# Kernel tuning notes

Measured on AMD Instinct MI355X. Metric: run time of the kernel, lower is better.

Reference implementation:

```python
import jax, jax.numpy as jnp
import numpy as np

DEPTH = 6
D_IN = 512
D_OUT = 256
NUM_NODES = 2 ** (DEPTH + 1) - 1   # 127
NUM_LEAVES = 2 ** (DEPTH + 1)      # 128
BATCH = 8192
EPS = 0.01


def _routes(depth):
    num_nodes = 2 ** (depth + 1) - 1
    num_leaves = 2 ** (depth + 1)
    idxs = np.zeros((num_leaves, depth + 1), np.int32)
    sides = np.zeros((num_leaves, depth + 1), np.int32)
    for i in range(num_leaves):
        temp, temp_sides = [], []
        leaf_idx = num_nodes + i
        for _ in range(depth):
            parent_idx = (leaf_idx - 1) // 2
            temp.append(parent_idx)
            temp_sides.append(1 if (leaf_idx - 1) % 2 == 0 else 0)
            leaf_idx = parent_idx
        temp_sides.append(1 if (leaf_idx - 1) % 2 == 0 else 0)
        temp.append(0)
        idxs[i] = temp[::-1]
        sides[i] = temp_sides[::-1]
    return idxs, sides


def _l2norm(v, axis):
    # matches torch F.normalize (eps=1e-12)
    n = jnp.sqrt(jnp.sum(v * v, axis=axis, keepdims=True))
    return v / jnp.maximum(n, 1e-12)


def setup_inputs() -> dict:
    key = jax.random.key(0)
    ks = jax.random.split(key, 6)
    D1 = D_IN + 1  # pre-network output dim
    x = jax.random.normal(ks[0], (BATCH, D_IN), jnp.float32)
    # pre_network Linear(D_IN, D_IN+1)
    W_pre = jax.random.normal(ks[1], (D1, D_IN), jnp.float32) * (1.0 / np.sqrt(D_IN))
    b_pre = jax.random.normal(ks[2], (D1,), jnp.float32) * 0.01
    # node hyperplanes [num_nodes, D1]
    right_w = jax.random.normal(ks[3], (NUM_NODES, D1), jnp.float32)
    # leaves Linear(D1, out*num_leaves)
    W_leaf = jax.random.normal(ks[4], (D_OUT * NUM_LEAVES, D1), jnp.float32) * (1.0 / np.sqrt(D1))
    b_leaf = jax.random.normal(ks[5], (D_OUT * NUM_LEAVES,), jnp.float32) * 0.01
    idxs, sides = _routes(DEPTH)
    return {
        "x": x, "W_pre": W_pre, "b_pre": b_pre, "right_w": right_w,
        "W_leaf": W_leaf, "b_leaf": b_leaf,
        "route_idx": jnp.asarray(idxs, jnp.int32),
        "route_side": jnp.asarray(sides, jnp.int32),
    }


def reference(x, W_pre, b_pre, right_w, W_leaf, b_leaf, route_idx, route_side):
    b = x.shape[0]
    # pre-network: Linear + ReLU  -> [b, D1]
    h = jax.nn.relu(x @ W_pre.T + b_pre)
    # node probabilities (cosine-similarity routing)
    nx = _l2norm(h, axis=1)                  # [b, D1]
    nw = _l2norm(right_w, axis=1)            # [N, D1]
    right = nx @ nw.T                        # [b, N]
    right_dist = (1.0 - right) / 2.0
    left_dist = 1.0 - right_dist
    # all_indices [2, N, b]
    all_ind = jnp.stack([right_dist.T, left_dist.T], axis=0)
    # gather route probs -> [L, depth+1, b]
    probs = all_ind[route_side, route_idx]
    log_probs = jnp.log(jnp.clip(probs, EPS, 1.0 - EPS))
    leaves_logp = jnp.sum(log_probs, axis=1)        # [L, b]
    s_w = jnp.exp(leaves_logp)                       # [L, b]
    entropy = -jnp.sum(s_w * leaves_logp, axis=0)    # [b]
    max_entropy = (NUM_LEAVES / DEPTH) * jnp.log(jnp.float32(DEPTH))
    entropy_loss = entropy / max_entropy
    # all leaf outputs at once -> [b, L, out]
    results = (h @ W_leaf.T + b_leaf).reshape(b, NUM_LEAVES, D_OUT)
    # NOTE: original multiplies by (randn(1) + 1 + entropy_loss.mean());
    # the randn(1) term is fixed to 0 for a deterministic reference.
    scale = 1.0 + jnp.mean(entropy_loss)
    out = jnp.sum(results * scale * s_w.T[:, :, None], axis=1)  # [b, out]
    return out
```

## Files before the change

kernel.cpp:

```cpp
#include <hip/hip_runtime.h>

typedef _Float16 f16;
typedef unsigned short u16;
typedef unsigned int u32;
typedef _Float16 f16x8 __attribute__((ext_vector_type(8)));
typedef float f32x4 __attribute__((ext_vector_type(4)));

union F16x8U { f16x8 v; uint4 q; u16 us[8]; f16 h[8]; };
union HBits { f16 f; u16 u; };

#define GLD16(g, l)                                                        \
  __builtin_amdgcn_global_load_lds(                                        \
      (const __attribute__((address_space(1))) void*)(g),                  \
      (__attribute__((address_space(3))) void*)(l), 16, 0, 0)

__global__ void kcvt_x(const float* __restrict__ x, f16* __restrict__ xo) {
  int i = (blockIdx.x * 256 + threadIdx.x) << 3;
  float4 a = *(const float4*)(x + i);
  float4 b = *(const float4*)(x + i + 4);
  F16x8U u;
  u.h[0] = (f16)a.x; u.h[1] = (f16)a.y; u.h[2] = (f16)a.z; u.h[3] = (f16)a.w;
  u.h[4] = (f16)b.x; u.h[5] = (f16)b.y; u.h[6] = (f16)b.z; u.h[7] = (f16)b.w;
  *(uint4*)(xo + i) = u.q;
}

__global__ void kcvt_wpre(const float* __restrict__ w, f16* __restrict__ wo) {
  int e = (blockIdx.x * 256 + threadIdx.x) << 2;
  int row = e >> 9, col = e & 511;
  union { uint2 q; f16 h[4]; } u;
  if (row < 513) {
    float4 v = *(const float4*)(w + (size_t)row * 512 + col);
    u.h[0] = (f16)v.x; u.h[1] = (f16)v.y; u.h[2] = (f16)v.z; u.h[3] = (f16)v.w;
  } else {
    u.h[0] = u.h[1] = u.h[2] = u.h[3] = (f16)0.0f;
  }
  *(uint2*)(wo + e) = u.q;
}

__global__ void kcvt_rw(const float* __restrict__ rwsrc, f16* __restrict__ ro) {
  int e = (blockIdx.x * 256 + threadIdx.x) << 2;
  int row = e / 576, c0 = e - row * 576;
  union { uint2 q; f16 h[4]; } u;
#pragma unroll
  for (int i = 0; i < 4; ++i) {
    int c = c0 + i;
    float v = (row < 127 && c < 513) ? rwsrc[(size_t)row * 513 + c] : 0.0f;
    u.h[i] = (f16)v;
  }
  *(uint2*)(ro + e) = u.q;
}

__global__ void kcvt_wleaf(const float* __restrict__ wl, const float* __restrict__ bl,
                           f16* __restrict__ wo) {
  int e = (blockIdx.x * 256 + threadIdx.x) << 3;
  int row = e / 544, c0 = e - row * 544;
  const float* src = wl + (size_t)row * 513 + c0;
  F16x8U u;
#pragma unroll
  for (int i = 0; i < 8; ++i) {
    int c = c0 + i;
    float v = (c < 513) ? src[i] : ((c == 513) ? bl[row] : 0.0f);
    u.h[i] = (f16)v;
  }
  *(uint4*)(wo + e) = u.q;
}

template <int MODE>
__global__ __launch_bounds__(256, 2) void kgemm(
    const f16* __restrict__ A, const f16* __restrict__ B,
    const float* __restrict__ bias, void* __restrict__ C,
    int NK, int astr, int bstr) {
  __shared__ alignas(16) f16 al[2][128 * 32];
  __shared__ alignas(16) f16 bl[2][64 * 40];
  const int tid = threadIdx.x, lane = tid & 63, wid = tid >> 6;
  const int wm = wid >> 1, wn = wid & 1;
  const int brow = blockIdx.x << 7, bcol = blockIdx.y << 6;

  int arow[2], aseg[2];
#pragma unroll
  for (int i = 0; i < 2; ++i) { int c = i * 256 + tid; arow[i] = c >> 2; aseg[i] = c & 3; }
  int br0 = tid / 5, bs0 = tid - br0 * 5;
  int c1 = 256 + lane;
  int br1 = c1 / 5, bs1 = c1 - br1 * 5;

  f32x4 acc[4][2];
#pragma unroll
  for (int mf = 0; mf < 4; ++mf)
#pragma unroll
    for (int nf = 0; nf < 2; ++nf)
#pragma unroll
      for (int j = 0; j < 4; ++j) acc[mf][nf][j] = 0.0f;

  auto stage = [&](int kc, int bf) {
    int kcol = kc << 5;
#pragma unroll
    for (int i = 0; i < 2; ++i) {
      f16* ldsb = &al[bf][(i * 256 + (wid << 6)) << 3];
      GLD16(A + (size_t)(brow + arow[i]) * astr + kcol + (aseg[i] << 3), ldsb);
    }
    {
      f16* ldsb = &bl[bf][(wid << 6) << 3];
      GLD16(B + (size_t)(bcol + br0) * bstr + kcol + (bs0 < 4 ? (bs0 << 3) : 0), ldsb);
    }
    if (wid == 0) {
      f16* ldsb = &bl[bf][256 << 3];
      GLD16(B + (size_t)(bcol + br1) * bstr + kcol + (bs1 < 4 ? (bs1 << 3) : 0), ldsb);
    }
  };

  stage(0, 0);
  __syncthreads();
  int cur = 0;
  for (int kc = 0; kc < NK; ++kc) {
    if (kc + 1 < NK) stage(kc + 1, cur ^ 1);
    f16x8 af[4], bfm[2];
#pragma unroll
    for (int mf = 0; mf < 4; ++mf)
      af[mf] = *(const f16x8*)&al[cur][((wm << 6) + (mf << 4) + (lane & 15)) * 32 + ((lane >> 4) << 3)];
#pragma unroll
    for (int nf = 0; nf < 2; ++nf)
      bfm[nf] = *(const f16x8*)&bl[cur][((wn << 5) + (nf << 4) + (lane & 15)) * 40 + ((lane >> 4) << 3)];
#pragma unroll
    for (int mf = 0; mf < 4; ++mf)
#pragma unroll
      for (int nf = 0; nf < 2; ++nf)
        acc[mf][nf] = __builtin_amdgcn_mfma_f32_16x16x32_f16(af[mf], bfm[nf], acc[mf][nf], 0, 0, 0);
    __syncthreads();
    cur ^= 1;
  }

#pragma unroll
  for (int mf = 0; mf < 4; ++mf) {
#pragma unroll
    for (int nf = 0; nf < 2; ++nf) {
      int gcol = bcol + (wn << 5) + (nf << 4) + (lane & 15);
      int gr0 = brow + (wm << 6) + (mf << 4) + ((lane >> 4) << 2);
      if (MODE == 0) {
        float bv = (gcol < 513) ? bias[gcol] : 0.0f;
#pragma unroll
        for (int j = 0; j < 4; ++j) {
          float v = fmaxf(acc[mf][nf][j] + bv, 0.0f);
          ((f16*)C)[(size_t)(gr0 + j) * 576 + gcol] = (gcol == 513) ? (f16)1.0f : (f16)v;
        }
      } else {
#pragma unroll
        for (int j = 0; j < 4; ++j)
          ((float*)C)[(size_t)(gr0 + j) * 128 + gcol] = acc[mf][nf][j];
      }
    }
  }
}

__global__ void khnorm(const f16* __restrict__ hf, float* __restrict__ ihn) {
  int row = (blockIdx.x << 2) + (threadIdx.x >> 6);
  int lane = threadIdx.x & 63;
  float s = 0.0f;
  for (int c = lane; c < 513; c += 64) {
    float v = (float)hf[(size_t)row * 576 + c];
    s += v * v;
  }
  for (int o = 32; o; o >>= 1) s += __shfl_down(s, o);
  if (!lane) ihn[row] = 1.0f / fmaxf(sqrtf(s), 1e-12f);
}

__global__ void kinvrw(const float* __restrict__ rw, float* __restrict__ irw) {
  int j = (blockIdx.x << 2) + (threadIdx.x >> 6);
  if (j >= 127) return;
  int lane = threadIdx.x & 63;
  float s = 0.0f;
  for (int d = lane; d < 513; d += 64) {
    float v = rw[(size_t)j * 513 + d];
    s += v * v;
  }
  for (int o = 32; o; o >>= 1) s += __shfl_down(s, o);
  if (!lane) irw[j] = 1.0f / fmaxf(sqrtf(s), 1e-12f);
}

__global__ void kroute(const float* __restrict__ G, const float* __restrict__ ihn,
                       const float* __restrict__ irw, u16* __restrict__ swh,
                       float* __restrict__ entp) {
  int b = blockIdx.x * 256 + threadIdx.x;
  float ih = ihn[b];
  const float* g = G + (size_t)b * 128;
  float ent = 0.0f;
  size_t wbase = (size_t)(b & ~127) + (((size_t)b & 15) << 3) + ((b >> 4) & 7);
  for (int l = 0; l < 128; ++l) {
    int n = 0;
    float lp = 0.0f;
#pragma unroll
    for (int k = 6; k >= 0; --k) {
      int bit = (l >> k) & 1;
      float cs = g[n] * ih * irw[n];
      float pr = bit ? 0.5f * (1.0f - cs) : 0.5f * (1.0f + cs);
      pr = fminf(fmaxf(pr, 0.01f), 0.99f);
      lp += __logf(pr);
      n = 2 * n + 1 + bit;
    }
    float sw = __expf(lp);
    ent -= sw * lp;
    HBits hb; hb.f = (f16)sw;
    swh[(size_t)l * 8192 + wbase] = hb.u;
  }
  for (int o = 32; o; o >>= 1) ent += __shfl_down(ent, o);
  __shared__ float red[4];
  if (!(threadIdx.x & 63)) red[threadIdx.x >> 6] = ent;
  __syncthreads();
  if (!threadIdx.x) atomicAdd(entp, red[0] + red[1] + red[2] + red[3]);
}

__global__ __launch_bounds__(512, 2) void kbig(
    const f16* __restrict__ hf, const f16* __restrict__ wp,
    const u16* __restrict__ swh, const float* __restrict__ entp,
    float* __restrict__ out) {
  __shared__ alignas(16) u16 slds[16384];
  __shared__ alignas(16) f16 blds[4][8192];

  const int tid = threadIdx.x;
  const int lane = tid & 63, wid = tid >> 6;
  const int lh = wid >> 2;
  const int wm = (wid >> 1) & 1;
  const int wn = wid & 1;

  const int d = blockIdx.x;
  const int ob = (d >> 1) & 3;
  const int mb = ((d & 1) << 5) | (d >> 3);
  const int brow = mb << 7;
  const int ocol = ob << 6;

#pragma unroll
  for (int i = 0; i < 4; ++i) {
    int c = i * 512 + tid;
    int l = c >> 4, q = (c & 15) << 3;
    GLD16(swh + ((size_t)l << 13) + brow + q, slds + ((i * 512 + (wid << 6)) << 3));
  }

  int pb[2];
#pragma unroll
  for (int i = 0; i < 2; ++i) {
    int c = i * 512 + tid;
    int leaf = c >> 8, r = (c >> 2) & 63, sl = c & 3;
    int ss = sl ^ ((r >> 2) & 3);
    pb[i] = (leaf * 256 + ocol + r) * 544 + (ss << 3);
  }
  auto stageB = [&](int s) {
    const f16* src = wp + (size_t)(s & 31) * 557056 + ((s >> 5) << 5);
    f16* bb = blds[s & 3];
#pragma unroll
    for (int i = 0; i < 2; ++i)
      GLD16(src + pb[i], bb + ((i * 512 + (wid << 6)) << 3));
  };

  stageB(0);
  stageB(1);

  f32x4 acc[4][2];
#pragma unroll
  for (int mf = 0; mf < 4; ++mf)
#pragma unroll
    for (int nf = 0; nf < 2; ++nf)
#pragma unroll
      for (int j = 0; j < 4; ++j) acc[mf][nf][j] = 0.0f;

  f16x8 afr[4];
  const f16* abase = hf + (size_t)(brow + (wm << 6) + (lane & 15)) * 576 + ((lane >> 4) << 3);
  int boff[2];
#pragma unroll
  for (int nf = 0; nf < 2; ++nf) {
    int r = (wn << 5) + (nf << 4) + (lane & 15);
    int s4 = (lane >> 4) ^ ((r >> 2) & 3);
    boff[nf] = (r << 5) + (s4 << 3);
  }
  const int soff = ((lane & 15) << 3) + (wm << 2);

  for (int s = 0; s < 544; ++s) {
    const int kc = s >> 5, lg = s & 31;
    if (lg == 0) {
      const f16* ap = abase + (kc << 5);
#pragma unroll
      for (int mf = 0; mf < 4; ++mf)
        afr[mf] = *(const f16x8*)(ap + (size_t)(mf << 4) * 576);
    }
    __builtin_amdgcn_sched_barrier(0);
    if (s + 2 < 544) stageB(s + 2);
    __builtin_amdgcn_sched_barrier(0);
    if (s + 2 < 544)      asm volatile("s_waitcnt vmcnt(4)" ::: "memory");
    else if (s == 542)    asm volatile("s_waitcnt vmcnt(2)" ::: "memory");
    else                  asm volatile("s_waitcnt vmcnt(0)" ::: "memory");
    __builtin_amdgcn_s_barrier();
    __builtin_amdgcn_sched_barrier(0);

    const f16* bb = blds[s & 3];
    __builtin_amdgcn_s_setprio(1);
#pragma unroll
    for (int ls = 0; ls < 2; ++ls) {
      const int l = (lg << 2) + (lh << 1) + ls;
      uint2 sq = *(const uint2*)(slds + (l << 7) + soff);
      const f16* bl0 = bb + ((l & 3) << 11);
      f16x8 bfr0 = *(const f16x8*)(bl0 + boff[0]);
      f16x8 bfr1 = *(const f16x8*)(bl0 + boff[1]);
      u16 sc[4] = {(u16)(sq.x & 0xffffu), (u16)(sq.x >> 16),
                   (u16)(sq.y & 0xffffu), (u16)(sq.y >> 16)};
#pragma unroll
      for (int mf = 0; mf < 4; ++mf) {
        HBits hb; hb.u = sc[mf];
        f16x8 as = afr[mf] * hb.f;
        acc[mf][0] = __builtin_amdgcn_mfma_f32_16x16x32_f16(as, bfr0, acc[mf][0], 0, 0, 0);
        acc[mf][1] = __builtin_amdgcn_mfma_f32_16x16x32_f16(as, bfr1, acc[mf][1], 0, 0, 0);
      }
    }
    __builtin_amdgcn_s_setprio(0);
    __builtin_amdgcn_sched_barrier(0);
  }

  float* rb = (float*)&blds[0][0];
  const int p = (wm << 1) | wn;
  if (lh == 1) {
    float* wbase = rb + ((p << 6) + lane) * 36;
#pragma unroll
    for (int mf = 0; mf < 4; ++mf)
#pragma unroll
      for (int nf = 0; nf < 2; ++nf)
        *(f32x4*)(wbase + (((mf << 1) + nf) << 2)) = acc[mf][nf];
  }
  __syncthreads();
  if (lh == 0) {
    const float* rbase = rb + ((p << 6) + lane) * 36;
    float ent = *entp;
    float scale = 1.0f + ent / (8192.0f * (128.0f / 6.0f) * logf(6.0f));
    const int cc0 = ocol + (wn << 5) + (lane & 15);
#pragma unroll
    for (int mf = 0; mf < 4; ++mf) {
#pragma unroll
      for (int nf = 0; nf < 2; ++nf) {
        f32x4 o = acc[mf][nf] + *(const f32x4*)(rbase + (((mf << 1) + nf) << 2));
        int r0 = brow + (wm << 6) + (mf << 4) + ((lane >> 4) << 2);
        int cc = cc0 + (nf << 4);
#pragma unroll
        for (int j = 0; j < 4; ++j)
          out[(size_t)(r0 + j) * 256 + cc] = scale * o[j];
      }
    }
  }
}

extern "C" void kernel_launch(void* const* d_in, const int* in_sizes, int n_in,
                              void* d_out, int out_size, void* d_ws, size_t ws_size,
                              hipStream_t stream) {
  const float* x     = (const float*)d_in[0];
  const float* wpre  = (const float*)d_in[1];
  const float* bpre  = (const float*)d_in[2];
  const float* rw    = (const float*)d_in[3];
  const float* wleaf = (const float*)d_in[4];
  const float* bleaf = (const float*)d_in[5];
  float* out = (float*)d_out;

  char* ws = (char*)d_ws;
  constexpr size_t O_ENT = 0;
  constexpr size_t O_XO  = 256;
  constexpr size_t O_WPO = O_XO  + 8388608;
  constexpr size_t O_RWO = O_WPO + 589824;
  constexpr size_t O_IRW = O_RWO + 147456;
  constexpr size_t O_HO  = O_IRW + 512;
  constexpr size_t O_IHN = O_HO  + 9437184;
  constexpr size_t O_G   = O_IHN + 32768;
  constexpr size_t O_SWH = O_G   + 4194304;
  constexpr size_t O_WPK = O_SWH + 2097152;

  float* ent = (float*)(ws + O_ENT);
  f16* xo   = (f16*)(ws + O_XO);
  f16* wpo  = (f16*)(ws + O_WPO);
  f16* rwo  = (f16*)(ws + O_RWO);
  float* irw = (float*)(ws + O_IRW);
  f16* ho   = (f16*)(ws + O_HO);
  float* ihn = (float*)(ws + O_IHN);
  float* go = (float*)(ws + O_G);
  u16* swh  = (u16*)(ws + O_SWH);
  f16* wpk  = (f16*)(ws + O_WPK);

  hipMemsetAsync(ent, 0, sizeof(float), stream);
  kcvt_x<<<2048, 256, 0, stream>>>(x, xo);
  kcvt_wpre<<<288, 256, 0, stream>>>(wpre, wpo);
  kcvt_rw<<<72, 256, 0, stream>>>(rw, rwo);
  kcvt_wleaf<<<8704, 256, 0, stream>>>(wleaf, bleaf, wpk);
  kgemm<0><<<dim3(64, 9), 256, 0, stream>>>(xo, wpo, bpre, (void*)ho, 16, 512, 512);
  khnorm<<<2048, 256, 0, stream>>>(ho, ihn);
  kinvrw<<<32, 256, 0, stream>>>(rw, irw);
  kgemm<1><<<dim3(64, 2), 256, 0, stream>>>(ho, rwo, nullptr, (void*)go, 17, 576, 576);
  kroute<<<32, 256, 0, stream>>>(go, ihn, irw, swh, ent);
  kbig<<<256, 512, 0, stream>>>(ho, wpk, swh, ent, out);
}
```

Before: 691.4 us.

## Restructure leaf GEMM with 32x32 MFMA, LDS-staged A, and split-leaf reduction

The main leaf-mixture kernel is rebuilt. Each of the 8 waves now handles a different leaf, using 32x32x16 MFMAs on a 128x32 output tile. The A operand is staged through LDS with global_load_lds instead of being read directly from global memory. Partial sums from the 8 waves are combined with a tree reduction in LDS. Grid size is doubled to 512 blocks with occupancy hint 4, the route-weight write layout is changed to match the new fragment mapping, and the four conversion kernels are merged into one launch. The goal is better MFMA efficiency and fewer launches, at the cost of a longer serialized reduction epilogue and more LDS per block.

```diff
diff --git a/kernel.cpp b/kernel.cpp
--- a/kernel.cpp
+++ b/kernel.cpp
@@ -5,6 +5,7 @@
 typedef unsigned int u32;
 typedef _Float16 f16x8 __attribute__((ext_vector_type(8)));
 typedef float f32x4 __attribute__((ext_vector_type(4)));
+typedef float f32x16 __attribute__((ext_vector_type(16)));
 
 union F16x8U { f16x8 v; uint4 q; u16 us[8]; f16 h[8]; };
 union HBits { f16 f; u16 u; };
@@ -14,55 +15,55 @@
       (const __attribute__((address_space(1))) void*)(g),                  \
       (__attribute__((address_space(3))) void*)(l), 16, 0, 0)
 
-__global__ void kcvt_x(const float* __restrict__ x, f16* __restrict__ xo) {
-  int i = (blockIdx.x * 256 + threadIdx.x) << 3;
-  float4 a = *(const float4*)(x + i);
-  float4 b = *(const float4*)(x + i + 4);
-  F16x8U u;
-  u.h[0] = (f16)a.x; u.h[1] = (f16)a.y; u.h[2] = (f16)a.z; u.h[3] = (f16)a.w;
-  u.h[4] = (f16)b.x; u.h[5] = (f16)b.y; u.h[6] = (f16)b.z; u.h[7] = (f16)b.w;
-  *(uint4*)(xo + i) = u.q;
-}
-
-__global__ void kcvt_wpre(const float* __restrict__ w, f16* __restrict__ wo) {
-  int e = (blockIdx.x * 256 + threadIdx.x) << 2;
-  int row = e >> 9, col = e & 511;
-  union { uint2 q; f16 h[4]; } u;
-  if (row < 513) {
-    float4 v = *(const float4*)(w + (size_t)row * 512 + col);
-    u.h[0] = (f16)v.x; u.h[1] = (f16)v.y; u.h[2] = (f16)v.z; u.h[3] = (f16)v.w;
+__global__ void kcvt_all(const float* __restrict__ x, f16* __restrict__ xo,
+                         const float* __restrict__ w, f16* __restrict__ wo,
+                         const float* __restrict__ rwsrc, f16* __restrict__ ro,
+                         const float* __restrict__ wl, const float* __restrict__ blf,
+                         f16* __restrict__ wpk) {
+  int b = blockIdx.x;
+  if (b < 2048) {
+    int i = (b * 256 + threadIdx.x) << 3;
+    float4 a = *(const float4*)(x + i);
+    float4 c = *(const float4*)(x + i + 4);
+    F16x8U u;
+    u.h[0] = (f16)a.x; u.h[1] = (f16)a.y; u.h[2] = (f16)a.z; u.h[3] = (f16)a.w;
+    u.h[4] = (f16)c.x; u.h[5] = (f16)c.y; u.h[6] = (f16)c.z; u.h[7] = (f16)c.w;
+    *(uint4*)(xo + i) = u.q;
+  } else if (b < 2336) {
+    int e = ((b - 2048) * 256 + threadIdx.x) << 2;
+    int row = e >> 9, col = e & 511;
+    union { uint2 q; f16 h[4]; } u;
+    if (row < 513) {
+      float4 v = *(const float4*)(w + (size_t)row * 512 + col);
+      u.h[0] = (f16)v.x; u.h[1] = (f16)v.y; u.h[2] = (f16)v.z; u.h[3] = (f16)v.w;
+    } else {
+      u.h[0] = u.h[1] = u.h[2] = u.h[3] = (f16)0.0f;
+    }
+    *(uint2*)(wo + e) = u.q;
+  } else if (b < 2408) {
+    int e = ((b - 2336) * 256 + threadIdx.x) << 2;
+    int row = e / 576, c0 = e - row * 576;
+    union { uint2 q; f16 h[4]; } u;
+#pragma unroll
+    for (int i = 0; i < 4; ++i) {
+      int c = c0 + i;
+      float v = (row < 127 && c < 513) ? rwsrc[(size_t)row * 513 + c] : 0.0f;
+      u.h[i] = (f16)v;
+    }
+    *(uint2*)(ro + e) = u.q;
   } else {
-    u.h[0] = u.h[1] = u.h[2] = u.h[3] = (f16)0.0f;
-  }
-  *(uint2*)(wo + e) = u.q;
-}
-
-__global__ void kcvt_rw(const float* __restrict__ rwsrc, f16* __restrict__ ro) {
-  int e = (blockIdx.x * 256 + threadIdx.x) << 2;
-  int row = e / 576, c0 = e - row * 576;
-  union { uint2 q; f16 h[4]; } u;
-#pragma unroll
-  for (int i = 0; i < 4; ++i) {
-    int c = c0 + i;
-    float v = (row < 127 && c < 513) ? rwsrc[(size_t)row * 513 + c] : 0.0f;
-    u.h[i] = (f16)v;
-  }
-  *(uint2*)(ro + e) = u.q;
-}
-
-__global__ void kcvt_wleaf(const float* __restrict__ wl, const float* __restrict__ bl,
-                           f16* __restrict__ wo) {
-  int e = (blockIdx.x * 256 + threadIdx.x) << 3;
-  int row = e / 544, c0 = e - row * 544;
-  const float* src = wl + (size_t)row * 513 + c0;
-  F16x8U u;
-#pragma unroll
-  for (int i = 0; i < 8; ++i) {
-    int c = c0 + i;
-    float v = (c < 513) ? src[i] : ((c == 513) ? bl[row] : 0.0f);
-    u.h[i] = (f16)v;
-  }
-  *(uint4*)(wo + e) = u.q;
+    int e = ((b - 2408) * 256 + threadIdx.x) << 3;
+    int row = e / 544, c0 = e - row * 544;
+    const float* src = wl + (size_t)row * 513 + c0;
+    F16x8U u;
+#pragma unroll
+    for (int i = 0; i < 8; ++i) {
+      int c = c0 + i;
+      float v = (c < 513) ? src[i] : ((c == 513) ? blf[row] : 0.0f);
+      u.h[i] = (f16)v;
+    }
+    *(uint4*)(wpk + e) = u.q;
+  }
 }
 
 template <int MODE>
@@ -183,7 +184,7 @@
   float ih = ihn[b];
   const float* g = G + (size_t)b * 128;
   float ent = 0.0f;
-  size_t wbase = (size_t)(b & ~127) + (((size_t)b & 15) << 3) + ((b >> 4) & 7);
+  size_t wbase = (size_t)(b & ~127) + (((b & 31) >> 1) << 3) + ((b & 1) << 2) + ((b >> 5) & 3);
   for (int l = 0; l < 128; ++l) {
     int n = 0;
     float lp = 0.0f;
@@ -208,138 +209,148 @@
   if (!threadIdx.x) atomicAdd(entp, red[0] + red[1] + red[2] + red[3]);
 }
 
-__global__ __launch_bounds__(512, 2) void kbig(
+__global__ __launch_bounds__(512, 4) void kbig(
     const f16* __restrict__ hf, const f16* __restrict__ wp,
     const u16* __restrict__ swh, const float* __restrict__ entp,
     float* __restrict__ out) {
-  __shared__ alignas(16) u16 slds[16384];
-  __shared__ alignas(16) f16 blds[4][8192];
-
-  const int tid = threadIdx.x;
-  const int lane = tid & 63, wid = tid >> 6;
-  const int lh = wid >> 2;
-  const int wm = (wid >> 1) & 1;
-  const int wn = wid & 1;
-
-  const int d = blockIdx.x;
-  const int ob = (d >> 1) & 3;
-  const int mb = ((d & 1) << 5) | (d >> 3);
-  const int brow = mb << 7;
-  const int ocol = ob << 6;
+  __shared__ alignas(16) char smem[73728];
+
+  const int tid = threadIdx.x, lane = tid & 63, wid = tid >> 6;
+  const int obl = blockIdx.x & 7, mb = blockIdx.x >> 3;
+  const int brow = mb << 7, ocol = obl << 5;
 
 #pragma unroll
   for (int i = 0; i < 4; ++i) {
     int c = i * 512 + tid;
-    int l = c >> 4, q = (c & 15) << 3;
-    GLD16(swh + ((size_t)l << 13) + brow + q, slds + ((i * 512 + (wid << 6)) << 3));
-  }
-
-  int pb[2];
-#pragma unroll
-  for (int i = 0; i < 2; ++i) {
-    int c = i * 512 + tid;
-    int leaf = c >> 8, r = (c >> 2) & 63, sl = c & 3;
-    int ss = sl ^ ((r >> 2) & 3);
-    pb[i] = (leaf * 256 + ocol + r) * 544 + (ss << 3);
-  }
-  auto stageB = [&](int s) {
-    const f16* src = wp + (size_t)(s & 31) * 557056 + ((s >> 5) << 5);
-    f16* bb = blds[s & 3];
-#pragma unroll
-    for (int i = 0; i < 2; ++i)
-      GLD16(src + pb[i], bb + ((i * 512 + (wid << 6)) << 3));
-  };
-
+    int l = c >> 4, rg = c & 15;
+    GLD16(swh + (size_t)l * 8192 + mb * 128 + rg * 8,
+          smem + ((i * 512 + (wid << 6)) << 4));
+  }
+  auto stageA = [&](int kcp) {
+    int c = tid & 255, q = c >> 7, row = c & 127;
+    GLD16(hf + (size_t)(brow + row) * 576 + kcp * 16 + q * 8,
+          smem + 65536 + ((kcp & 1) << 12) + ((wid & 3) << 10));
+  };
+  auto stageB = [&](int s2) {
+    int kcp = s2 >> 4, lgp = s2 & 15;
+    int col = lane & 31, q = (lane >> 5) & 1;
+    GLD16(wp + (size_t)((lgp * 8 + wid) * 256 + ocol + col) * 544 + kcp * 16 + q * 8,
+          smem + 32768 + ((s2 & 3) << 13) + (wid << 10));
+  };
+  stageA(0);
   stageB(0);
   stageB(1);
 
-  f32x4 acc[4][2];
+  f32x16 acc[4];
 #pragma unroll
   for (int mf = 0; mf < 4; ++mf)
 #pragma unroll
-    for (int nf = 0; nf < 2; ++nf)
-#pragma unroll
-      for (int j = 0; j < 4; ++j) acc[mf][nf][j] = 0.0f;
+    for (int j = 0; j < 16; ++j) acc[mf][j] = 0.0f;
 
   f16x8 afr[4];
-  const f16* abase = hf + (size_t)(brow + (wm << 6) + (lane & 15)) * 576 + ((lane >> 4) << 3);
-  int boff[2];
-#pragma unroll
-  for (int nf = 0; nf < 2; ++nf) {
-    int r = (wn << 5) + (nf << 4) + (lane & 15);
-    int s4 = (lane >> 4) ^ ((r >> 2) & 3);
-    boff[nf] = (r << 5) + (s4 << 3);
-  }
-  const int soff = ((lane & 15) << 3) + (wm << 2);
-
-  for (int s = 0; s < 544; ++s) {
-    const int kc = s >> 5, lg = s & 31;
-    if (lg == 0) {
-      const f16* ap = abase + (kc << 5);
-#pragma unroll
-      for (int mf = 0; mf < 4; ++mf)
-        afr[mf] = *(const f16x8*)(ap + (size_t)(mf << 4) * 576);
-    }
-    __builtin_amdgcn_sched_barrier(0);
-    if (s + 2 < 544) stageB(s + 2);
-    __builtin_amdgcn_sched_barrier(0);
-    if (s + 2 < 544)      asm volatile("s_waitcnt vmcnt(4)" ::: "memory");
-    else if (s == 542)    asm volatile("s_waitcnt vmcnt(2)" ::: "memory");
-    else                  asm volatile("s_waitcnt vmcnt(0)" ::: "memory");
-    __builtin_amdgcn_s_barrier();
-    __builtin_amdgcn_sched_barrier(0);
-
-    const f16* bb = blds[s & 3];
-    __builtin_amdgcn_s_setprio(1);
-#pragma unroll
-    for (int ls = 0; ls < 2; ++ls) {
-      const int l = (lg << 2) + (lh << 1) + ls;
-      uint2 sq = *(const uint2*)(slds + (l << 7) + soff);
-      const f16* bl0 = bb + ((l & 3) << 11);
-      f16x8 bfr0 = *(const f16x8*)(bl0 + boff[0]);
-      f16x8 bfr1 = *(const f16x8*)(bl0 + boff[1]);
-      u16 sc[4] = {(u16)(sq.x & 0xffffu), (u16)(sq.x >> 16),
-                   (u16)(sq.y & 0xffffu), (u16)(sq.y >> 16)};
+  const int aoff = 65536 + ((lane >> 5) << 11) + ((lane & 31) << 4);
+  const int boff = 32768 + (wid << 10) + ((lane >> 5) << 9) + ((lane & 31) << 4);
+  const int swoff = ((lane & 31) << 3);
+
+  for (int kc = 0; kc < 33; ++kc) {
+#pragma unroll
+    for (int lg = 0; lg < 16; ++lg) {
+      const int s = kc * 16 + lg;
+      stageB(s + 2);
+      if (lg == 4) stageA(kc + 1);
+      if (lg >= 4 && lg <= 6) asm volatile("s_waitcnt vmcnt(3)" ::: "memory");
+      else                    asm volatile("s_waitcnt vmcnt(2)" ::: "memory");
+      __builtin_amdgcn_s_barrier();
+      __builtin_amdgcn_sched_barrier(0);
+      if (lg == 0) {
+#pragma unroll
+        for (int mf = 0; mf < 4; ++mf)
+          afr[mf] = *(const f16x8*)(smem + aoff + ((kc & 1) << 12) + (mf << 9));
+      }
+      const int l = lg * 8 + wid;
+      uint2 swq = *(const uint2*)(smem + (l << 8) + swoff);
+      f16x8 bfr = *(const f16x8*)(smem + boff + ((s & 3) << 13));
+      const u16* sc = (const u16*)&swq;
+      __builtin_amdgcn_s_setprio(1);
 #pragma unroll
       for (int mf = 0; mf < 4; ++mf) {
         HBits hb; hb.u = sc[mf];
         f16x8 as = afr[mf] * hb.f;
-        acc[mf][0] = __builtin_amdgcn_mfma_f32_16x16x32_f16(as, bfr0, acc[mf][0], 0, 0, 0);
-        acc[mf][1] = __builtin_amdgcn_mfma_f32_16x16x32_f16(as, bfr1, acc[mf][1], 0, 0, 0);
-      }
-    }
-    __builtin_amdgcn_s_setprio(0);
-    __builtin_amdgcn_sched_barrier(0);
-  }
-
-  float* rb = (float*)&blds[0][0];
-  const int p = (wm << 1) | wn;
-  if (lh == 1) {
-    float* wbase = rb + ((p << 6) + lane) * 36;
-#pragma unroll
-    for (int mf = 0; mf < 4; ++mf)
-#pragma unroll
-      for (int nf = 0; nf < 2; ++nf)
-        *(f32x4*)(wbase + (((mf << 1) + nf) << 2)) = acc[mf][nf];
-  }
-  __syncthreads();
-  if (lh == 0) {
-    const float* rbase = rb + ((p << 6) + lane) * 36;
-    float ent = *entp;
-    float scale = 1.0f + ent / (8192.0f * (128.0f / 6.0f) * logf(6.0f));
-    const int cc0 = ocol + (wn << 5) + (lane & 15);
-#pragma unroll
-    for (int mf = 0; mf < 4; ++mf) {
-#pragma unroll
-      for (int nf = 0; nf < 2; ++nf) {
-        f32x4 o = acc[mf][nf] + *(const f32x4*)(rbase + (((mf << 1) + nf) << 2));
-        int r0 = brow + (wm << 6) + (mf << 4) + ((lane >> 4) << 2);
-        int cc = cc0 + (nf << 4);
-#pragma unroll
-        for (int j = 0; j < 4; ++j)
-          out[(size_t)(r0 + j) * 256 + cc] = scale * o[j];
-      }
-    }
+        acc[mf] = __builtin_amdgcn_mfma_f32_32x32x16_f16(as, bfr, acc[mf], 0, 0, 0);
+      }
+      __builtin_amdgcn_s_setprio(0);
+      __builtin_amdgcn_sched_barrier(0);
+    }
+  }
+  {
+    const int kc = 33;
+#pragma unroll
+    for (int lg = 0; lg < 16; ++lg) {
+      const int s = kc * 16 + lg;
+      if (lg <= 13) stageB(s + 2);
+      if (lg <= 13)      asm volatile("s_waitcnt vmcnt(2)" ::: "memory");
+      else if (lg == 14) asm volatile("s_waitcnt vmcnt(1)" ::: "memory");
+      else               asm volatile("s_waitcnt vmcnt(0)" ::: "memory");
+      __builtin_amdgcn_s_barrier();
+      __builtin_amdgcn_sched_barrier(0);
+      if (lg == 0) {
+#pragma unroll
+        for (int mf = 0; mf < 4; ++mf)
+          afr[mf] = *(const f16x8*)(smem + aoff + ((kc & 1) << 12) + (mf << 9));
+      }
+      const int l = lg * 8 + wid;
+      uint2 swq = *(const uint2*)(smem + (l << 8) + swoff);
+      f16x8 bfr = *(const f16x8*)(smem + boff + ((s & 3) << 13));
+      const u16* sc = (const u16*)&swq;
+      __builtin_amdgcn_s_setprio(1);
+#pragma unroll
+      for (int mf = 0; mf < 4; ++mf) {
+        HBits hb; hb.u = sc[mf];
+        f16x8 as = afr[mf] * hb.f;
+        acc[mf] = __builtin_amdgcn_mfma_f32_32x32x16_f16(as, bfr, acc[mf], 0, 0, 0);
+      }
+      __builtin_amdgcn_s_setprio(0);
+      __builtin_amdgcn_sched_barrier(0);
+    }
+  }
+
+  auto writeAcc = [&](char* base) {
+#pragma unroll
+    for (int mf = 0; mf < 4; ++mf)
+#pragma unroll
+      for (int rq = 0; rq < 4; ++rq)
+        *(f32x4*)(base + ((((mf << 2) + rq) << 6) + lane) * 16) =
+            ((const f32x4*)&acc[mf])[rq];
+  };
+  auto addAcc = [&](const char* base) {
+#pragma unroll
+    for (int mf = 0; mf < 4; ++mf)
+#pragma unroll
+      for (int rq = 0; rq < 4; ++rq) {
+        f32x4 v = *(const f32x4*)(base + ((((mf << 2) + rq) << 6) + lane) * 16);
+        ((f32x4*)&acc[mf])[rq] += v;
+      }
+  };
+  if (wid >= 4) writeAcc(smem + ((wid - 4) << 14));
+  __syncthreads();
+  if (wid < 4) addAcc(smem + (wid << 14));
+  __syncthreads();
+  if (wid == 2 || wid == 3) writeAcc(smem + ((wid - 2) << 14));
+  __syncthreads();
+  if (wid < 2) addAcc(smem + (wid << 14));
+  __syncthreads();
+  if (wid == 1) writeAcc(smem);
+  __syncthreads();
+  if (wid == 0) {
+    addAcc(smem);
+    float scale = 1.0f + (*entp) / (8192.0f * (128.0f / 6.0f) * logf(6.0f));
+#pragma unroll
+    for (int mf = 0; mf < 4; ++mf)
+#pragma unroll
+      for (int r = 0; r < 16; ++r) {
+        int row = brow + (mf << 5) + (r & 3) + ((r >> 2) << 3) + ((lane >> 5) << 2);
+        out[(size_t)row * 256 + ocol + (lane & 31)] = scale * acc[mf][r];
+      }
   }
 }
 
@@ -378,14 +389,11 @@
   f16* wpk  = (f16*)(ws + O_WPK);
 
   hipMemsetAsync(ent, 0, sizeof(float), stream);
-  kcvt_x<<<2048, 256, 0, stream>>>(x, xo);
-  kcvt_wpre<<<288, 256, 0, stream>>>(wpre, wpo);
-  kcvt_rw<<<72, 256, 0, stream>>>(rw, rwo);
-  kcvt_wleaf<<<8704, 256, 0, stream>>>(wleaf, bleaf, wpk);
+  kcvt_all<<<11112, 256, 0, stream>>>(x, xo, wpre, wpo, rw, rwo, wleaf, bleaf, wpk);
   kgemm<0><<<dim3(64, 9), 256, 0, stream>>>(xo, wpo, bpre, (void*)ho, 16, 512, 512);
   khnorm<<<2048, 256, 0, stream>>>(ho, ihn);
   kinvrw<<<32, 256, 0, stream>>>(rw, irw);
   kgemm<1><<<dim3(64, 2), 256, 0, stream>>>(ho, rwo, nullptr, (void*)go, 17, 576, 576);
   kroute<<<32, 256, 0, stream>>>(go, ihn, irw, swh, ent);
-  kbig<<<256, 512, 0, stream>>>(ho, wpk, swh, ent, out);
-}
+  kbig<<<512, 512, 0, stream>>>(ho, wpk, swh, ent, out);
+}
```

Measured after the change: 654.5 us. 1.06x faster.
